# Kernel optimization log

Measured on AMD Instinct MI355X. Metric: run time of the kernel, lower is better.

The kernel has to match this reference:

```python
import jax, jax.numpy as jnp
import numpy as np

NH, NKV, HD, PD = 16, 4, 128, 16  # heads, kv heads, head dim, rotary partial dim
BASE = 10000.0
QK_GAIN_INIT = 5.25


def _rms_norm(x):
    # F.rms_norm over last dim, eps = dtype eps (torch default when eps=None)
    return x * jax.lax.rsqrt(jnp.mean(x * x, axis=-1, keepdims=True) + jnp.finfo(x.dtype).eps)


def _rope_partial(x, cos, sin):
    # rotate first PD dims (two halves of PD//2), pass through the rest
    h = PD // 2
    x1, x2, xp = x[..., :h], x[..., h:PD], x[..., PD:]
    return jnp.concatenate([x1 * cos + x2 * sin, -x2 * cos + x1 * sin, xp], axis=-1)


def setup_inputs() -> dict:
    key = jax.random.key(0)
    ks = jax.random.split(key, 5)
    B, T, D = 2, 2048, 2048
    KD = NKV * HD
    s = 0.02
    return {
        "x": jax.random.normal(ks[0], (B, T, D), jnp.float32),
        "wq": jax.random.normal(ks[1], (D, D), jnp.float32) * s,
        "wk": jax.random.normal(ks[2], (KD, D), jnp.float32) * s,
        "wv": jax.random.normal(ks[3], (KD, D), jnp.float32) * s,
        "wp": jax.random.normal(ks[4], (D, D), jnp.float32) * s,
        "qg": jnp.full((NH,), QK_GAIN_INIT, jnp.float32),
    }


def reference(x, wq, wk, wv, wp, qg):
    B, T, D = x.shape
    q = (x @ wq.T).reshape(B, T, NH, HD)    # [B,T,NH,HD]
    k = (x @ wk.T).reshape(B, T, NKV, HD)   # [B,T,NKV,HD]
    v = (x @ wv.T).reshape(B, T, NKV, HD)
    q = _rms_norm(q)
    k = _rms_norm(k)
    # partial rotary tables: [T, PD//2] -> broadcast over head dim
    t = jnp.arange(T, dtype=jnp.float32)
    inv = 1.0 / (BASE ** (jnp.arange(0, PD, 2, dtype=jnp.float32) / PD))
    f = t[:, None] * inv[None, :]
    cos, sin = jnp.cos(f)[:, None, :], jnp.sin(f)[:, None, :]  # [T,1,PD//2]
    q = _rope_partial(q, cos, sin)
    k = _rope_partial(k, cos, sin)
    q = q * qg[None, None, :, None]         # learned per-head QK gain
    scale = 1.0 / jnp.sqrt(jnp.float32(HD))
    G = NH // NKV
    qh = q.reshape(B, T, NKV, G, HD)
    scores = jnp.einsum('bqkgd,bskd->bkgqs', qh, k) * scale  # [B,NKV,G,T,T]
    causal = jnp.arange(T)[:, None] >= jnp.arange(T)[None, :]
    scores = jnp.where(causal[None, None, None], scores, -jnp.inf)
    p = jax.nn.softmax(scores, axis=-1)
    y = jnp.einsum('bkgqs,bskd->bqkgd', p, v).reshape(B, T, D)
    return y @ wp.T
```

## Files before the change

### kernel.cpp

```cpp
#include <hip/hip_runtime.h>
#include <hip/hip_bf16.h>

#define B_   2
#define T_   2048
#define D_   2048
#define NH_  16
#define NKV_ 4
#define HD_  128
#define KD_  512
#define BT_  4096

typedef __bf16 bf16x8 __attribute__((ext_vector_type(8)));
typedef float  f32x4  __attribute__((ext_vector_type(4)));
typedef float  f32x16 __attribute__((ext_vector_type(16)));

__device__ __forceinline__ void gload_lds16(const __hip_bfloat16* g, __hip_bfloat16* l) {
    __builtin_amdgcn_global_load_lds(
        (__attribute__((address_space(1))) void*)(g),
        (__attribute__((address_space(3))) void*)(l),
        16, 0, 0);
}

__global__ void f2b_all(const float4* __restrict__ x,  const float4* __restrict__ wq,
                        const float4* __restrict__ wk, const float4* __restrict__ wv,
                        const float4* __restrict__ wp,
                        ushort4* __restrict__ xb,  ushort4* __restrict__ wqb,
                        ushort4* __restrict__ wkb, ushort4* __restrict__ wvb,
                        ushort4* __restrict__ wpb) {
    const int e0 = BT_ * D_ / 4;
    const int e1 = e0 + D_ * D_ / 4;
    const int e2 = e1 + KD_ * D_ / 4;
    const int e3 = e2 + KD_ * D_ / 4;
    const int e4 = e3 + D_ * D_ / 4;
    int idx = blockIdx.x * blockDim.x + threadIdx.x;
    int stride = gridDim.x * blockDim.x;
    for (int j = idx; j < e4; j += stride) {
        const float4* src; ushort4* dst; int off;
        if      (j < e0) { src = x;  dst = xb;  off = j; }
        else if (j < e1) { src = wq; dst = wqb; off = j - e0; }
        else if (j < e2) { src = wk; dst = wkb; off = j - e1; }
        else if (j < e3) { src = wv; dst = wvb; off = j - e2; }
        else             { src = wp; dst = wpb; off = j - e3; }
        float4 v = src[off];
        __hip_bfloat16 a = __float2bfloat16(v.x), b = __float2bfloat16(v.y),
                       c = __float2bfloat16(v.z), d = __float2bfloat16(v.w);
        ushort4 o;
        o.x = *(const unsigned short*)&a; o.y = *(const unsigned short*)&b;
        o.z = *(const unsigned short*)&c; o.w = *(const unsigned short*)&d;
        dst[off] = o;
    }
}

#define GEMM_TILE_BODY(Aptr, Bptr, Cptr, colL, Nc, K)                                         \
    const int tid = threadIdx.x, w = tid >> 6, lane = tid & 63;                               \
    const int lr = lane & 15, lk = lane >> 4;                                                 \
    const int wr = w >> 1, wc = w & 1;                                                        \
    const size_t row0 = (size_t)blockIdx.x * 128;                                             \
    const __hip_bfloat16* ga = (Aptr) + (row0 + tid / 4) * (K) + (tid % 4) * 8;               \
    const __hip_bfloat16* gb = (Bptr) + ((size_t)(colL) + tid / 4) * (K) + (tid % 4) * 8;     \
    const int KI = (K) >> 5;                                                                  \
    auto stage = [&](int u) {                                                                 \
        int uu = u < KI ? u : KI - 1;                                                         \
        const int kk = uu * 32;                                                               \
        const int slot = u & 3;                                                               \
        gload_lds16(ga + kk,                  &As[slot][w * 512]);                            \
        gload_lds16(ga + kk + (size_t)64*(K), &As[slot][2048 + w * 512]);                     \
        gload_lds16(gb + kk,                  &Bs[slot][w * 512]);                            \
        gload_lds16(gb + kk + (size_t)64*(K), &Bs[slot][2048 + w * 512]);                     \
    };                                                                                        \
    f32x4 acc[4][4] = {};                                                                     \
    stage(0); stage(1);                                                                       \
    for (int kt = 0; kt < KI; ++kt) {                                                         \
        stage(kt + 2);                                                                        \
        asm volatile("s_waitcnt vmcnt(8)" ::: "memory");                                      \
        __builtin_amdgcn_s_barrier();                                                         \
        __builtin_amdgcn_sched_barrier(0);                                                    \
        const int slot = kt & 3;                                                              \
        bf16x8 af[4], bfr[4];                                                                 \
        _Pragma("unroll")                                                                     \
        for (int m = 0; m < 4; m++)                                                           \
            af[m] = *(const bf16x8*)&As[slot][(wr * 64 + m * 16 + lr) * 32 + lk * 8];         \
        _Pragma("unroll")                                                                     \
        for (int n = 0; n < 4; n++)                                                           \
            bfr[n] = *(const bf16x8*)&Bs[slot][(wc * 64 + n * 16 + lr) * 32 + lk * 8];        \
        _Pragma("unroll")                                                                     \
        for (int m = 0; m < 4; m++)                                                           \
            _Pragma("unroll")                                                                 \
            for (int n = 0; n < 4; n++)                                                       \
                acc[m][n] = __builtin_amdgcn_mfma_f32_16x16x32_bf16(af[m], bfr[n],            \
                                                                    acc[m][n], 0, 0, 0);      \
    }                                                                                         \
    _Pragma("unroll")                                                                         \
    for (int m = 0; m < 4; m++)                                                               \
        _Pragma("unroll")                                                                     \
        for (int n = 0; n < 4; n++)                                                           \
            _Pragma("unroll")                                                                 \
            for (int r = 0; r < 4; r++)                                                       \
                (Cptr)[(row0 + wr * 64 + m * 16 + lk * 4 + r) * (Nc)                          \
                       + (colL) + wc * 64 + n * 16 + lr] = acc[m][n][r];

__global__ __launch_bounds__(256, 2)
void gemm_qkv(const __hip_bfloat16* __restrict__ A,
              const __hip_bfloat16* __restrict__ Wq, const __hip_bfloat16* __restrict__ Wk,
              const __hip_bfloat16* __restrict__ Wv,
              float* __restrict__ Cq, float* __restrict__ Ck, float* __restrict__ Cv) {
    __shared__ __attribute__((aligned(16))) __hip_bfloat16 As[4][4096];
    __shared__ __attribute__((aligned(16))) __hip_bfloat16 Bs[4][4096];
    const int cb = blockIdx.y;
    const __hip_bfloat16* Bw; float* Cm; int Nc, colL;
    if (cb < 16)      { Bw = Wq; Cm = Cq; Nc = D_;  colL = cb * 128; }
    else if (cb < 20) { Bw = Wk; Cm = Ck; Nc = KD_; colL = (cb - 16) * 128; }
    else              { Bw = Wv; Cm = Cv; Nc = KD_; colL = (cb - 20) * 128; }
    GEMM_TILE_BODY(A, Bw, Cm, colL, Nc, D_)
}

__global__ __launch_bounds__(256, 2)
void gemm_p(const __hip_bfloat16* __restrict__ A, const __hip_bfloat16* __restrict__ B,
            float* __restrict__ C, int N, int K) {
    __shared__ __attribute__((aligned(16))) __hip_bfloat16 As[4][4096];
    __shared__ __attribute__((aligned(16))) __hip_bfloat16 Bs[4][4096];
    const int colL = blockIdx.y * 128;
    GEMM_TILE_BODY(A, B, C, colL, N, K)
}

__global__ __launch_bounds__(256)
void norm_rope(const float* __restrict__ qf, const float* __restrict__ kf, const float* __restrict__ vf,
               const float* __restrict__ qg,
               __hip_bfloat16* __restrict__ qb, __hip_bfloat16* __restrict__ kb, __hip_bfloat16* __restrict__ vb) {
    int wid  = (blockIdx.x * 256 + threadIdx.x) >> 6;
    int lane = threadIdx.x & 63;
    int bt = wid / 24, hh = wid % 24;
    int b = bt >> 11, t = bt & (T_ - 1);

    const float* row;
    if (hh < NH_)            row = qf + (size_t)bt * D_  + hh * HD_;
    else if (hh < NH_+NKV_)  row = kf + (size_t)bt * KD_ + (hh - NH_) * HD_;
    else                     row = vf + (size_t)bt * KD_ + (hh - NH_ - NKV_) * HD_;

    float2 xv = *(const float2*)(row + lane * 2);

    if (hh >= NH_ + NKV_) {
        int kv = hh - NH_ - NKV_;
        __hip_bfloat16* o = vb + ((size_t)(b * NKV_ + kv) * T_ + t) * HD_ + lane * 2;
        o[0] = __float2bfloat16(xv.x); o[1] = __float2bfloat16(xv.y);
        return;
    }

    float ss = xv.x * xv.x + xv.y * xv.y;
    #pragma unroll
    for (int off = 32; off; off >>= 1) ss += __shfl_xor(ss, off);
    float rn = rsqrtf(ss * (1.0f / HD_) + 1.1920929e-7f);
    float y0 = xv.x * rn, y1 = xv.y * rn;

    float py0 = __shfl_xor(y0, 4), py1 = __shfl_xor(y1, 4);
    float o0 = y0, o1 = y1;
    if (lane < 8) {
        int i0 = (2 * lane) & 7;
        float f0 = (float)t * exp2f(-(float)i0       * 1.66096404744368f);
        float f1 = (float)t * exp2f(-(float)(i0 + 1) * 1.66096404744368f);
        float s0, c0, s1, c1;
        sincosf(f0, &s0, &c0);
        sincosf(f1, &s1, &c1);
        if (lane < 4) { o0 =  y0 * c0 + py0 * s0; o1 =  y1 * c1 + py1 * s1; }
        else          { o0 = -y0 * c0 + py0 * s0; o1 = -y1 * c1 + py1 * s1; }
    }

    if (hh < NH_) {
        float g = qg[hh] * 0.1275174305f;
        o0 *= g; o1 *= g;
        __hip_bfloat16* o = qb + ((size_t)(b * NH_ + hh) * T_ + t) * HD_ + lane * 2;
        o[0] = __float2bfloat16(o0); o[1] = __float2bfloat16(o1);
    } else {
        int kv = hh - NH_;
        __hip_bfloat16* o = kb + ((size_t)(b * NKV_ + kv) * T_ + t) * HD_ + lane * 2;
        o[0] = __float2bfloat16(o0); o[1] = __float2bfloat16(o1);
    }
}

__global__ void vtrans(const __hip_bfloat16* __restrict__ vb, __hip_bfloat16* __restrict__ vt) {
    __shared__ __hip_bfloat16 tile[32][33];
    int bk = blockIdx.z;
    int t0 = blockIdx.x * 32, h0 = blockIdx.y * 32;
    int tx = threadIdx.x, ty = threadIdx.y;
    const __hip_bfloat16* src = vb + ((size_t)bk * T_ + t0) * HD_ + h0;
    #pragma unroll
    for (int j = 0; j < 4; j++) tile[ty + j * 8][tx] = src[(size_t)(ty + j * 8) * HD_ + tx];
    __syncthreads();
    __hip_bfloat16* dst = vt + ((size_t)bk * HD_ + h0) * T_ + t0;
    #pragma unroll
    for (int j = 0; j < 4; j++) dst[(size_t)(ty + j * 8) * T_ + tx] = tile[tx][ty + j * 8];
}

__device__ __forceinline__ unsigned pkbf(float a, float b) {
    __hip_bfloat16 x = __float2bfloat16(a), y = __float2bfloat16(b);
    unsigned short xu = *(const unsigned short*)&x, yu = *(const unsigned short*)&y;
    return (unsigned)xu | ((unsigned)yu << 16);
}

union U8u { unsigned u[4]; bf16x8 v; };

__global__ __launch_bounds__(512, 2)
void attn_fwd(const __hip_bfloat16* __restrict__ qb, const __hip_bfloat16* __restrict__ kb,
              const __hip_bfloat16* __restrict__ vt, __hip_bfloat16* __restrict__ yb) {
    __shared__ __attribute__((aligned(16))) __hip_bfloat16 Ks[2][4][4096];
    __shared__ __attribute__((aligned(16))) __hip_bfloat16 Vs[2][4][4096];
    const int tid  = threadIdx.x;
    const int w    = tid >> 6, lane = tid & 63;
    const int l31  = lane & 31, hi = lane >> 5;
    const int hd4  = w & 3;
    const int seg  = w >> 2;
    const int bid  = blockIdx.x;
    const int strm = bid & 7;
    const int b    = strm >> 2, kvh = strm & 3;
    const int idx  = bid >> 3;
    const int c    = (idx < 32) ? (63 - 2 * idx) : (126 - 2 * idx);
    const int ns   = (c >> 1) + 1;
    const int h    = kvh * 4 + hd4;
    const int qa   = c * 32;

    const __hip_bfloat16* qp = qb + ((size_t)(b * NH_ + h) * T_ + qa) * HD_;
    const __hip_bfloat16* kp = kb + (size_t)(b * NKV_ + kvh) * T_ * HD_;
    const __hip_bfloat16* vp = vt + (size_t)(b * NKV_ + kvh) * HD_ * T_;

    const int tt = tid & 255, sg = tid >> 8;
    const int k_hs = tt >> 5, k_kv = tt & 31;
    const int v_kg = tt >> 7, v_d  = tt & 127;
    const __hip_bfloat16* ksrc0 = kp + (size_t)k_kv * HD_ + k_hs * 8;
    const __hip_bfloat16* ksrc1 = kp + (size_t)k_kv * HD_ + (8 + k_hs) * 8;
    const __hip_bfloat16* vsrc0 = vp + (size_t)v_d * T_ + v_kg * 8;
    const __hip_bfloat16* vsrc1 = vp + (size_t)v_d * T_ + (2 + v_kg) * 8;

    auto stage = [&](int u) {
        int kt0 = u < ns - 1 ? u : ns - 1;
        int kt1 = ns + u; if (kt1 > c) kt1 = c;
        const int kvb = (sg ? kt1 : kt0) * 32;
        const int slot = u & 3;
        __hip_bfloat16* kd = &Ks[sg][slot][(tt >> 6) * 512];
        __hip_bfloat16* vd = &Vs[sg][slot][(tt >> 6) * 512];
        gload_lds16(ksrc0 + (size_t)kvb * HD_, kd);
        gload_lds16(ksrc1 + (size_t)kvb * HD_, kd + 2048);
        gload_lds16(vsrc0 + kvb,               vd);
        gload_lds16(vsrc1 + kvb,               vd + 2048);
    };

    bf16x8 qfr[8];
    #pragma unroll
    for (int hb = 0; hb < 8; ++hb)
        qfr[hb] = *(const bf16x8*)(qp + (size_t)l31 * HD_ + hb * 16 + hi * 8);

    f32x16 o0 = {}, o1 = {}, o2 = {}, o3 = {};
    float m = -1e30f, s = 0.f;

    stage(0);
    stage(1);

    for (int t = 0; t < ns; ++t) {
        stage(t + 2);
        asm volatile("s_waitcnt vmcnt(8)" ::: "memory");
        __builtin_amdgcn_s_barrier();
        __builtin_amdgcn_sched_barrier(0);

        const int kt_raw = seg ? ns + t : t;
        const bool dead  = kt_raw > c;
        const int kt     = dead ? c : kt_raw;

        const __hip_bfloat16* Kb = &Ks[seg][t & 3][0];
        const __hip_bfloat16* Vb = &Vs[seg][t & 3][0];

        f32x16 sa_a = {}, sa_b = {};
        __builtin_amdgcn_s_setprio(1);
        #pragma unroll
        for (int hb = 0; hb < 4; ++hb) {
            bf16x8 kf = *(const bf16x8*)&Kb[((hb * 2 + hi) * 32 + l31) * 8];
            sa_a = __builtin_amdgcn_mfma_f32_32x32x16_bf16(kf, qfr[hb], sa_a, 0, 0, 0);
        }
        #pragma unroll
        for (int hb = 4; hb < 8; ++hb) {
            bf16x8 kf = *(const bf16x8*)&Kb[((hb * 2 + hi) * 32 + l31) * 8];
            sa_b = __builtin_amdgcn_mfma_f32_32x32x16_bf16(kf, qfr[hb], sa_b, 0, 0, 0);
        }
        __builtin_amdgcn_s_setprio(0);
        f32x16 sa = sa_a + sa_b;

        if (dead) {
            #pragma unroll
            for (int r = 0; r < 16; ++r) sa[r] = -1e30f;
        } else if (kt == c) {
            #pragma unroll
            for (int r = 0; r < 16; ++r) {
                int kvrel = (r & 3) + 8 * (r >> 2) + 4 * hi;
                if (kvrel > l31) sa[r] = -1e30f;
            }
        }
        float pm = sa[0];
        #pragma unroll
        for (int r = 1; r < 16; ++r) pm = fmaxf(pm, sa[r]);
        pm = fmaxf(pm, __shfl_xor(pm, 32));
        if (!__all(pm <= m + 8.f)) {
            float mn = fmaxf(m, pm);
            float corr = exp2f(m - mn);
            s *= corr;
            #pragma unroll
            for (int r = 0; r < 16; ++r) { o0[r] *= corr; o1[r] *= corr; o2[r] *= corr; o3[r] *= corr; }
            m = mn;
        }
        float p[16]; float rs = 0.f;
        #pragma unroll
        for (int r = 0; r < 16; ++r) { p[r] = exp2f(sa[r] - m); rs += p[r]; }
        rs += __shfl_xor(rs, 32);
        s += rs;
        unsigned pk[8];
        #pragma unroll
        for (int jj = 0; jj < 8; ++jj) pk[jj] = pkbf(p[2 * jj], p[2 * jj + 1]);
        unsigned pks[8];
        #pragma unroll
        for (int jj = 0; jj < 8; ++jj) pks[jj] = (unsigned)__shfl_xor((int)pk[jj], 32);
        U8u pa0, pa1;
        pa0.u[0] = hi ? pks[2] : pk[0];
        pa0.u[1] = hi ? pks[3] : pk[1];
        pa0.u[2] = hi ? pk[2]  : pks[0];
        pa0.u[3] = hi ? pk[3]  : pks[1];
        pa1.u[0] = hi ? pks[6] : pk[4];
        pa1.u[1] = hi ? pks[7] : pk[5];
        pa1.u[2] = hi ? pk[6]  : pks[4];
        pa1.u[3] = hi ? pk[7]  : pks[5];
        __builtin_amdgcn_s_setprio(1);
        #define PV_BLK(ON, DBLK)                                                              \
            {                                                                                 \
                bf16x8 vf0 = *(const bf16x8*)&Vb[((0 + hi) * 128 + (DBLK) * 32 + l31) * 8];   \
                bf16x8 vf1 = *(const bf16x8*)&Vb[((2 + hi) * 128 + (DBLK) * 32 + l31) * 8];   \
                ON = __builtin_amdgcn_mfma_f32_32x32x16_bf16(vf0, pa0.v, ON, 0, 0, 0);        \
                ON = __builtin_amdgcn_mfma_f32_32x32x16_bf16(vf1, pa1.v, ON, 0, 0, 0);        \
            }
        PV_BLK(o0, 0) PV_BLK(o1, 1) PV_BLK(o2, 2) PV_BLK(o3, 3)
        #undef PV_BLK
        __builtin_amdgcn_s_setprio(0);
    }

    asm volatile("s_waitcnt vmcnt(0)" ::: "memory");
    __syncthreads();
    float* Mh = (hd4 < 2) ? ((float*)&Ks[0][0][0] + hd4 * 4352)
                          : ((float*)&Vs[0][0][0] + (hd4 - 2) * 4352);
    if (seg == 1) {
        #pragma unroll
        for (int r = 0; r < 16; ++r) {
            Mh[(0 * 16 + r) * 64 + lane] = o0[r];
            Mh[(1 * 16 + r) * 64 + lane] = o1[r];
            Mh[(2 * 16 + r) * 64 + lane] = o2[r];
            Mh[(3 * 16 + r) * 64 + lane] = o3[r];
        }
        Mh[4096 + lane] = m;
        Mh[4160 + lane] = s;
    }
    __syncthreads();
    if (seg == 0) {
        float m1 = Mh[4096 + lane], s1 = Mh[4160 + lane];
        float mn = fmaxf(m, m1);
        float ca = exp2f(m - mn), cb = exp2f(m1 - mn);
        s = s * ca + s1 * cb;
        #pragma unroll
        for (int r = 0; r < 16; ++r) {
            o0[r] = o0[r] * ca + Mh[(0 * 16 + r) * 64 + lane] * cb;
            o1[r] = o1[r] * ca + Mh[(1 * 16 + r) * 64 + lane] * cb;
            o2[r] = o2[r] * ca + Mh[(2 * 16 + r) * 64 + lane] * cb;
            o3[r] = o3[r] * ca + Mh[(3 * 16 + r) * 64 + lane] * cb;
        }
        float inv = 1.0f / s;
        __hip_bfloat16* yrow = yb + ((size_t)b * T_ + qa + l31) * D_ + h * HD_;
        #define WRITE_DB(ON, DB)                                                        \
            _Pragma("unroll")                                                           \
            for (int r4 = 0; r4 < 4; ++r4) {                                            \
                ushort4 u;                                                              \
                __hip_bfloat16 e0 = __float2bfloat16(ON[4*r4+0] * inv);                 \
                __hip_bfloat16 e1 = __float2bfloat16(ON[4*r4+1] * inv);                 \
                __hip_bfloat16 e2 = __float2bfloat16(ON[4*r4+2] * inv);                 \
                __hip_bfloat16 e3 = __float2bfloat16(ON[4*r4+3] * inv);                 \
                u.x = *(const unsigned short*)&e0; u.y = *(const unsigned short*)&e1;   \
                u.z = *(const unsigned short*)&e2; u.w = *(const unsigned short*)&e3;   \
                *(ushort4*)(yrow + (DB) * 32 + 8 * r4 + 4 * hi) = u;                    \
            }
        WRITE_DB(o0, 0) WRITE_DB(o1, 1) WRITE_DB(o2, 2) WRITE_DB(o3, 3)
        #undef WRITE_DB
    }
}

extern "C" void kernel_launch(void* const* d_in, const int* in_sizes, int n_in,
                              void* d_out, int out_size, void* d_ws, size_t ws_size,
                              hipStream_t stream) {
    (void)in_sizes; (void)n_in; (void)out_size; (void)ws_size;
    const float* x  = (const float*)d_in[0];
    const float* wq = (const float*)d_in[1];
    const float* wk = (const float*)d_in[2];
    const float* wv = (const float*)d_in[3];
    const float* wp = (const float*)d_in[4];
    const float* qg = (const float*)d_in[5];
    float* out = (float*)d_out;

    char* ws = (char*)d_ws;
    size_t off = 0;
    auto alloc = [&](size_t bytes) { char* p = ws + off; off += (bytes + 255) & ~(size_t)255; return p; };

    __hip_bfloat16* xb  = (__hip_bfloat16*)alloc((size_t)BT_ * D_ * 2);
    __hip_bfloat16* wqb = (__hip_bfloat16*)alloc((size_t)D_ * D_ * 2);
    __hip_bfloat16* wkb = (__hip_bfloat16*)alloc((size_t)KD_ * D_ * 2);
    __hip_bfloat16* wvb = (__hip_bfloat16*)alloc((size_t)KD_ * D_ * 2);
    __hip_bfloat16* wpb = (__hip_bfloat16*)alloc((size_t)D_ * D_ * 2);
    float* qf = (float*)alloc((size_t)BT_ * D_ * 4);
    float* kf = (float*)alloc((size_t)BT_ * KD_ * 4);
    float* vf = (float*)alloc((size_t)BT_ * KD_ * 4);
    __hip_bfloat16* qbb = (__hip_bfloat16*)alloc((size_t)BT_ * D_ * 2);
    __hip_bfloat16* kbb = (__hip_bfloat16*)alloc((size_t)BT_ * KD_ * 2);
    __hip_bfloat16* ybb = xb;
    __hip_bfloat16* vbb = wqb;
    __hip_bfloat16* vtb = wqb + (size_t)B_ * NKV_ * T_ * HD_;

    f2b_all<<<2048, 256, 0, stream>>>((const float4*)x, (const float4*)wq, (const float4*)wk,
                                      (const float4*)wv, (const float4*)wp,
                                      (ushort4*)xb, (ushort4*)wqb, (ushort4*)wkb,
                                      (ushort4*)wvb, (ushort4*)wpb);

    dim3 gqkv(BT_ / 128, 24);
    gemm_qkv<<<gqkv, 256, 0, stream>>>(xb, wqb, wkb, wvb, qf, kf, vf);

    norm_rope<<<(BT_ * 24) / 4, 256, 0, stream>>>(qf, kf, vf, qg, qbb, kbb, vbb);

    dim3 gt(T_ / 32, HD_ / 32, B_ * NKV_);
    vtrans<<<gt, dim3(32, 8), 0, stream>>>(vbb, vtb);

    attn_fwd<<<512, 512, 0, stream>>>(qbb, kbb, vtb, ybb);

    dim3 gq(BT_ / 128, D_ / 128);
    gemm_p<<<gq, 256, 0, stream>>>(ybb, wpb, out, D_, D_);
}
```

Baseline: 235.4 us.

## Pre-swizzle K and V into MFMA fragment layout and load directly to registers

```diff
diff --git a/kernel.cpp b/kernel.cpp
--- a/kernel.cpp
+++ b/kernel.cpp
@@ -126,7 +126,7 @@
 __global__ __launch_bounds__(256)
 void norm_rope(const float* __restrict__ qf, const float* __restrict__ kf, const float* __restrict__ vf,
                const float* __restrict__ qg,
-               __hip_bfloat16* __restrict__ qb, __hip_bfloat16* __restrict__ kb, __hip_bfloat16* __restrict__ vb) {
+               __hip_bfloat16* __restrict__ qb, __hip_bfloat16* __restrict__ kfb, __hip_bfloat16* __restrict__ vb) {
     int wid  = (blockIdx.x * 256 + threadIdx.x) >> 6;
     int lane = threadIdx.x & 63;
     int bt = wid / 24, hh = wid % 24;
@@ -172,23 +172,38 @@
         o[0] = __float2bfloat16(o0); o[1] = __float2bfloat16(o1);
     } else {
         int kv = hh - NH_;
-        __hip_bfloat16* o = kb + ((size_t)(b * NKV_ + kv) * T_ + t) * HD_ + lane * 2;
+        int hb  = lane >> 3;
+        int hi2 = (lane >> 2) & 1;
+        int j   = (2 * lane) & 7;
+        size_t idxe = (size_t)(b * NKV_ + kv) * T_ * HD_
+                    + (size_t)((((t >> 5) * 8 + hb) * 2 + hi2)) * 256 + (t & 31) * 8 + j;
+        __hip_bfloat16* o = kfb + idxe;
         o[0] = __float2bfloat16(o0); o[1] = __float2bfloat16(o1);
     }
 }
 
-__global__ void vtrans(const __hip_bfloat16* __restrict__ vb, __hip_bfloat16* __restrict__ vt) {
+__global__ void vfrag_k(const __hip_bfloat16* __restrict__ vb, __hip_bfloat16* __restrict__ vfb) {
     __shared__ __hip_bfloat16 tile[32][33];
     int bk = blockIdx.z;
-    int t0 = blockIdx.x * 32, h0 = blockIdx.y * 32;
+    int t0 = blockIdx.x * 32, d0 = blockIdx.y * 32;
     int tx = threadIdx.x, ty = threadIdx.y;
-    const __hip_bfloat16* src = vb + ((size_t)bk * T_ + t0) * HD_ + h0;
+    const __hip_bfloat16* src = vb + ((size_t)bk * T_ + t0) * HD_ + d0;
     #pragma unroll
     for (int j = 0; j < 4; j++) tile[ty + j * 8][tx] = src[(size_t)(ty + j * 8) * HD_ + tx];
     __syncthreads();
-    __hip_bfloat16* dst = vt + ((size_t)bk * HD_ + h0) * T_ + t0;
-    #pragma unroll
-    for (int j = 0; j < 4; j++) dst[(size_t)(ty + j * 8) * T_ + tx] = tile[tx][ty + j * 8];
+    if (ty < 4) {
+        int sect = ty, l31 = tx;
+        ushort4 u0, u1;
+        unsigned short* up0 = (unsigned short*)&u0;
+        unsigned short* up1 = (unsigned short*)&u1;
+        #pragma unroll
+        for (int j = 0; j < 4; j++) up0[j] = *(const unsigned short*)&tile[sect * 8 + j][l31];
+        #pragma unroll
+        for (int j = 0; j < 4; j++) up1[j] = *(const unsigned short*)&tile[sect * 8 + 4 + j][l31];
+        ushort4* dst = (ushort4*)(vfb + (size_t)bk * T_ * HD_
+                     + (size_t)((((blockIdx.x * 4 + blockIdx.y) * 4 + sect) * 32 + l31)) * 8);
+        dst[0] = u0; dst[1] = u1;
+    }
 }
 
 __device__ __forceinline__ unsigned pkbf(float a, float b) {
@@ -200,10 +215,9 @@
 union U8u { unsigned u[4]; bf16x8 v; };
 
 __global__ __launch_bounds__(512, 2)
-void attn_fwd(const __hip_bfloat16* __restrict__ qb, const __hip_bfloat16* __restrict__ kb,
-              const __hip_bfloat16* __restrict__ vt, __hip_bfloat16* __restrict__ yb) {
-    __shared__ __attribute__((aligned(16))) __hip_bfloat16 Ks[2][4][4096];
-    __shared__ __attribute__((aligned(16))) __hip_bfloat16 Vs[2][4][4096];
+void attn_fwd(const __hip_bfloat16* __restrict__ qb, const __hip_bfloat16* __restrict__ kfb,
+              const __hip_bfloat16* __restrict__ vfb, __hip_bfloat16* __restrict__ yb) {
+    __shared__ float Mrg[4][4224];
     const int tid  = threadIdx.x;
     const int w    = tid >> 6, lane = tid & 63;
     const int l31  = lane & 31, hi = lane >> 5;
@@ -218,30 +232,9 @@
     const int h    = kvh * 4 + hd4;
     const int qa   = c * 32;
 
-    const __hip_bfloat16* qp = qb + ((size_t)(b * NH_ + h) * T_ + qa) * HD_;
-    const __hip_bfloat16* kp = kb + (size_t)(b * NKV_ + kvh) * T_ * HD_;
-    const __hip_bfloat16* vp = vt + (size_t)(b * NKV_ + kvh) * HD_ * T_;
-
-    const int tt = tid & 255, sg = tid >> 8;
-    const int k_hs = tt >> 5, k_kv = tt & 31;
-    const int v_kg = tt >> 7, v_d  = tt & 127;
-    const __hip_bfloat16* ksrc0 = kp + (size_t)k_kv * HD_ + k_hs * 8;
-    const __hip_bfloat16* ksrc1 = kp + (size_t)k_kv * HD_ + (8 + k_hs) * 8;
-    const __hip_bfloat16* vsrc0 = vp + (size_t)v_d * T_ + v_kg * 8;
-    const __hip_bfloat16* vsrc1 = vp + (size_t)v_d * T_ + (2 + v_kg) * 8;
-
-    auto stage = [&](int u) {
-        int kt0 = u < ns - 1 ? u : ns - 1;
-        int kt1 = ns + u; if (kt1 > c) kt1 = c;
-        const int kvb = (sg ? kt1 : kt0) * 32;
-        const int slot = u & 3;
-        __hip_bfloat16* kd = &Ks[sg][slot][(tt >> 6) * 512];
-        __hip_bfloat16* vd = &Vs[sg][slot][(tt >> 6) * 512];
-        gload_lds16(ksrc0 + (size_t)kvb * HD_, kd);
-        gload_lds16(ksrc1 + (size_t)kvb * HD_, kd + 2048);
-        gload_lds16(vsrc0 + kvb,               vd);
-        gload_lds16(vsrc1 + kvb,               vd + 2048);
-    };
+    const __hip_bfloat16* qp  = qb  + ((size_t)(b * NH_ + h) * T_ + qa) * HD_;
+    const __hip_bfloat16* kfp = kfb + (size_t)(b * NKV_ + kvh) * T_ * HD_ + lane * 8;
+    const __hip_bfloat16* vfp = vfb + (size_t)(b * NKV_ + kvh) * T_ * HD_ + lane * 8;
 
     bf16x8 qfr[8];
     #pragma unroll
@@ -251,36 +244,41 @@
     f32x16 o0 = {}, o1 = {}, o2 = {}, o3 = {};
     float m = -1e30f, s = 0.f;
 
-    stage(0);
-    stage(1);
+    bf16x8 kk[8], vv[8];
+    {
+        int kt0 = seg ? (ns <= c ? ns : c) : 0;
+        #pragma unroll
+        for (int hb = 0; hb < 8; ++hb)
+            kk[hb] = *(const bf16x8*)(kfp + ((size_t)kt0 * 16 + hb * 2) * 256);
+    }
 
     for (int t = 0; t < ns; ++t) {
-        stage(t + 2);
-        asm volatile("s_waitcnt vmcnt(8)" ::: "memory");
         __builtin_amdgcn_s_barrier();
-        __builtin_amdgcn_sched_barrier(0);
 
         const int kt_raw = seg ? ns + t : t;
         const bool dead  = kt_raw > c;
         const int kt     = dead ? c : kt_raw;
 
-        const __hip_bfloat16* Kb = &Ks[seg][t & 3][0];
-        const __hip_bfloat16* Vb = &Vs[seg][t & 3][0];
-
-        f32x16 sa_a = {}, sa_b = {};
+        #pragma unroll
+        for (int db = 0; db < 4; ++db) {
+            vv[db * 2]     = *(const bf16x8*)(vfp + ((size_t)kt * 16 + db * 4) * 256);
+            vv[db * 2 + 1] = *(const bf16x8*)(vfp + ((size_t)kt * 16 + db * 4) * 256 + 512);
+        }
+
+        f32x16 sa = {};
         __builtin_amdgcn_s_setprio(1);
         #pragma unroll
-        for (int hb = 0; hb < 4; ++hb) {
-            bf16x8 kf = *(const bf16x8*)&Kb[((hb * 2 + hi) * 32 + l31) * 8];
-            sa_a = __builtin_amdgcn_mfma_f32_32x32x16_bf16(kf, qfr[hb], sa_a, 0, 0, 0);
-        }
-        #pragma unroll
-        for (int hb = 4; hb < 8; ++hb) {
-            bf16x8 kf = *(const bf16x8*)&Kb[((hb * 2 + hi) * 32 + l31) * 8];
-            sa_b = __builtin_amdgcn_mfma_f32_32x32x16_bf16(kf, qfr[hb], sa_b, 0, 0, 0);
-        }
+        for (int hb = 0; hb < 8; ++hb)
+            sa = __builtin_amdgcn_mfma_f32_32x32x16_bf16(kk[hb], qfr[hb], sa, 0, 0, 0);
         __builtin_amdgcn_s_setprio(0);
-        f32x16 sa = sa_a + sa_b;
+
+        {
+            int ktn_r = (seg ? ns : 0) + t + 1;
+            int ktn = ktn_r > c ? c : ktn_r;
+            #pragma unroll
+            for (int hb = 0; hb < 8; ++hb)
+                kk[hb] = *(const bf16x8*)(kfp + ((size_t)ktn * 16 + hb * 2) * 256);
+        }
 
         if (dead) {
             #pragma unroll
@@ -325,22 +323,19 @@
         pa1.u[2] = hi ? pk[6]  : pks[4];
         pa1.u[3] = hi ? pk[7]  : pks[5];
         __builtin_amdgcn_s_setprio(1);
-        #define PV_BLK(ON, DBLK)                                                              \
-            {                                                                                 \
-                bf16x8 vf0 = *(const bf16x8*)&Vb[((0 + hi) * 128 + (DBLK) * 32 + l31) * 8];   \
-                bf16x8 vf1 = *(const bf16x8*)&Vb[((2 + hi) * 128 + (DBLK) * 32 + l31) * 8];   \
-                ON = __builtin_amdgcn_mfma_f32_32x32x16_bf16(vf0, pa0.v, ON, 0, 0, 0);        \
-                ON = __builtin_amdgcn_mfma_f32_32x32x16_bf16(vf1, pa1.v, ON, 0, 0, 0);        \
-            }
-        PV_BLK(o0, 0) PV_BLK(o1, 1) PV_BLK(o2, 2) PV_BLK(o3, 3)
-        #undef PV_BLK
+        o0 = __builtin_amdgcn_mfma_f32_32x32x16_bf16(vv[0], pa0.v, o0, 0, 0, 0);
+        o0 = __builtin_amdgcn_mfma_f32_32x32x16_bf16(vv[1], pa1.v, o0, 0, 0, 0);
+        o1 = __builtin_amdgcn_mfma_f32_32x32x16_bf16(vv[2], pa0.v, o1, 0, 0, 0);
+        o1 = __builtin_amdgcn_mfma_f32_32x32x16_bf16(vv[3], pa1.v, o1, 0, 0, 0);
+        o2 = __builtin_amdgcn_mfma_f32_32x32x16_bf16(vv[4], pa0.v, o2, 0, 0, 0);
+        o2 = __builtin_amdgcn_mfma_f32_32x32x16_bf16(vv[5], pa1.v, o2, 0, 0, 0);
+        o3 = __builtin_amdgcn_mfma_f32_32x32x16_bf16(vv[6], pa0.v, o3, 0, 0, 0);
+        o3 = __builtin_amdgcn_mfma_f32_32x32x16_bf16(vv[7], pa1.v, o3, 0, 0, 0);
         __builtin_amdgcn_s_setprio(0);
     }
 
-    asm volatile("s_waitcnt vmcnt(0)" ::: "memory");
     __syncthreads();
-    float* Mh = (hd4 < 2) ? ((float*)&Ks[0][0][0] + hd4 * 4352)
-                          : ((float*)&Vs[0][0][0] + (hd4 - 2) * 4352);
+    float* Mh = &Mrg[hd4][0];
     if (seg == 1) {
         #pragma unroll
         for (int r = 0; r < 16; ++r) {
@@ -409,10 +404,10 @@
     float* kf = (float*)alloc((size_t)BT_ * KD_ * 4);
     float* vf = (float*)alloc((size_t)BT_ * KD_ * 4);
     __hip_bfloat16* qbb = (__hip_bfloat16*)alloc((size_t)BT_ * D_ * 2);
-    __hip_bfloat16* kbb = (__hip_bfloat16*)alloc((size_t)BT_ * KD_ * 2);
+    __hip_bfloat16* kfb = (__hip_bfloat16*)alloc((size_t)BT_ * KD_ * 2);
+    __hip_bfloat16* vfb = (__hip_bfloat16*)alloc((size_t)BT_ * KD_ * 2);
     __hip_bfloat16* ybb = xb;
     __hip_bfloat16* vbb = wqb;
-    __hip_bfloat16* vtb = wqb + (size_t)B_ * NKV_ * T_ * HD_;
 
     f2b_all<<<2048, 256, 0, stream>>>((const float4*)x, (const float4*)wq, (const float4*)wk,
                                       (const float4*)wv, (const float4*)wp,
@@ -422,12 +417,12 @@
     dim3 gqkv(BT_ / 128, 24);
     gemm_qkv<<<gqkv, 256, 0, stream>>>(xb, wqb, wkb, wvb, qf, kf, vf);
 
-    norm_rope<<<(BT_ * 24) / 4, 256, 0, stream>>>(qf, kf, vf, qg, qbb, kbb, vbb);
+    norm_rope<<<(BT_ * 24) / 4, 256, 0, stream>>>(qf, kf, vf, qg, qbb, kfb, vbb);
 
     dim3 gt(T_ / 32, HD_ / 32, B_ * NKV_);
-    vtrans<<<gt, dim3(32, 8), 0, stream>>>(vbb, vtb);
-
-    attn_fwd<<<512, 512, 0, stream>>>(qbb, kbb, vtb, ybb);
+    vfrag_k<<<gt, dim3(32, 8), 0, stream>>>(vbb, vfb);
+
+    attn_fwd<<<512, 512, 0, stream>>>(qbb, kfb, vfb, ybb);
 
     dim3 gq(BT_ / 128, D_ / 128);
     gemm_p<<<gq, 256, 0, stream>>>(ybb, wpb, out, D_, D_);
```

Measured after the change: 236.8 us. About the same (+0.6%).
